# Kernel optimization log

Hardware: AMD Instinct MI355X
Metric: run time of the kernel (lower is better)

The kernel has to match this reference:

```python
import jax, jax.numpy as jnp
import numpy as np

D = 512      # n_embd
H = 8        # n_head
L = 2        # n_layer (per stack)
T = 2048     # sequence length / block_size
B = 1        # batch
BANDS = (999, 9)  # band_width for [phase, tool] stacks
EPS = 1e-5


def _sinusoidal(n_pos, dim):
    pos = np.arange(n_pos)[:, None].astype(np.float64)
    j = np.arange(dim)[None, :]
    angle = pos / np.power(10000.0, 2 * (j // 2) / dim)
    out = np.zeros((n_pos, dim), np.float32)
    out[:, 0::2] = np.sin(angle[:, 0::2])
    out[:, 1::2] = np.cos(angle[:, 1::2])
    return jnp.asarray(out)


def setup_inputs() -> dict:
    key = jax.random.key(0)
    ks = jax.random.split(key, 8)
    s = 0.02
    rn = lambda k, shp: jax.random.normal(k, shp, jnp.float32) * s
    inp = {
        "x": jax.random.normal(ks[0], (B, T, D), jnp.float32),
        "pos_emb": _sinusoidal(T, D),            # sinusoidal, frozen
        # leading dim 2 = [phase stack, tool stack], then layer dim L
        "ln1_w": jnp.ones((2, L, D)), "ln1_b": jnp.zeros((2, L, D)),
        "ln2_w": jnp.ones((2, L, D)), "ln2_b": jnp.zeros((2, L, D)),
        "Wq": rn(ks[1], (2, L, D, D)), "bq": jnp.zeros((2, L, D)),
        "Wk": rn(ks[2], (2, L, D, D)), "bk": jnp.zeros((2, L, D)),
        "Wv": rn(ks[3], (2, L, D, D)), "bv": jnp.zeros((2, L, D)),
        "Wo": rn(ks[4], (2, L, D, D)), "bo": jnp.zeros((2, L, D)),
        "W1": rn(ks[5], (2, L, D, 2 * D)), "b1": jnp.zeros((2, L, 2 * D)),
        "W2": rn(ks[6], (2, L, 2 * D, D)), "b2": jnp.zeros((2, L, D)),
        "lnf_w": jnp.ones((D,)), "lnf_b": jnp.zeros((D,)),
    }
    return inp


def _ln(x, w, b):
    mu = x.mean(-1, keepdims=True)
    var = ((x - mu) ** 2).mean(-1, keepdims=True)
    return (x - mu) / jnp.sqrt(var + EPS) * w + b


def _attn(x, Wq, bq, Wk, bk, Wv, bv, Wo, bo, bw):
    Bx, Tx, _ = x.shape
    Dh = D // H
    heads = lambda W, b: (x @ W + b).reshape(Bx, Tx, H, Dh).transpose(0, 2, 1, 3)
    q, k, v = heads(Wq, bq), heads(Wk, bk), heads(Wv, bv)
    att = jnp.einsum('bhqd,bhkd->bhqk', q, k) / jnp.sqrt(jnp.float32(Dh))
    i = jnp.arange(Tx)[:, None]
    j = jnp.arange(Tx)[None, :]
    mask = (j <= i) & (j >= i - bw)  # causal band
    att = jnp.where(mask, att, -jnp.inf)
    att = jax.nn.softmax(att, axis=-1)
    y = jnp.einsum('bhqk,bhkd->bhqd', att, v).transpose(0, 2, 1, 3).reshape(Bx, Tx, D)
    return y @ Wo + bo


def reference(x, pos_emb, ln1_w, ln1_b, ln2_w, ln2_b,
              Wq, bq, Wk, bk, Wv, bv, Wo, bo,
              W1, b1, W2, b2, lnf_w, lnf_b):
    Tx = x.shape[1]
    h0 = x + pos_emb[None, :Tx]
    outs = []
    for s in range(2):  # phase stack, tool stack
        bw = BANDS[s]
        h = h0
        for l in range(L):
            h = h + _attn(_ln(h, ln1_w[s, l], ln1_b[s, l]),
                          Wq[s, l], bq[s, l], Wk[s, l], bk[s, l],
                          Wv[s, l], bv[s, l], Wo[s, l], bo[s, l], bw)
            hm = _ln(h, ln2_w[s, l], ln2_b[s, l])
            h = h + (jax.nn.gelu(hm @ W1[s, l] + b1[s, l], approximate=False)
                     @ W2[s, l] + b2[s, l])
        outs.append(_ln(h, lnf_w, lnf_b))
    return (outs[0], outs[1])
```

## Files before the change

### kernel.cpp

```cpp
#include <hip/hip_runtime.h>
#include <stdint.h>

#define T 2048
#define D 512
#define NH 8
#define DH 64
#define L 2

typedef float floatx4 __attribute__((ext_vector_type(4)));
typedef short shortx8 __attribute__((ext_vector_type(8)));
typedef unsigned short u16;
typedef unsigned short u16x4 __attribute__((ext_vector_type(4)));

__device__ __forceinline__ u16 f2bf(float f) {
    union { float f; uint32_t u; } c; c.f = f;
    uint32_t u = c.u;
    u += 0x7fffu + ((u >> 16) & 1u);
    return (u16)(u >> 16);
}

__device__ __forceinline__ float bf2f(u16 v) {
    union { uint32_t u; float f; } c; c.u = ((uint32_t)v) << 16;
    return c.f;
}

__device__ __forceinline__ void load_lds16(const void* g, void* l) {
    __builtin_amdgcn_global_load_lds((const __attribute__((address_space(1))) void*)g,
                                     (__attribute__((address_space(3))) void*)l,
                                     16, 0, 0);
}

struct TransJobs {
    const float* src[6];
    u16* dst[6];
    const float* x;
    const float* pos;
    u16* h;
};

__global__ __launch_bounds__(256) void pre_kernel(TransJobs j) {
    __shared__ float tile[32][33];
    int tid = threadIdx.x;
    if (blockIdx.z == 24) {
        int idx = (blockIdx.y * 32 + blockIdx.x) * 256 + tid;
        float4 xv = ((const float4*)j.x)[idx];
        float4 pv = ((const float4*)j.pos)[idx];
        u16x4 hh;
        hh[0] = f2bf(xv.x + pv.x); hh[1] = f2bf(xv.y + pv.y);
        hh[2] = f2bf(xv.z + pv.z); hh[3] = f2bf(xv.w + pv.w);
        ((u16x4*)j.h)[idx] = hh;
        ((u16x4*)j.h)[idx + (T * D / 4)] = hh;
        return;
    }
    int m = blockIdx.z >> 2, slice = blockIdx.z & 3;
    int R = (m == 5) ? 1024 : 512;
    int C = (m == 4) ? 1024 : 512;
    if (blockIdx.x * 32 >= C || blockIdx.y * 32 >= R) return;
    const float* in = j.src[m] + (size_t)slice * R * C;
    u16* out = j.dst[m] + (size_t)slice * R * C;
    int tx = tid & 31, ty = tid >> 5;
    int x = blockIdx.x * 32 + tx;
    int y0 = blockIdx.y * 32;
#pragma unroll
    for (int i = 0; i < 4; i++)
        tile[ty + i * 8][tx] = in[(size_t)(y0 + ty + i * 8) * C + x];
    __syncthreads();
    int ox = y0 + tx;
#pragma unroll
    for (int i = 0; i < 4; i++)
        out[(size_t)(blockIdx.x * 32 + ty + i * 8) * R + ox] = f2bf(tile[tx][ty + i * 8]);
}

__global__ __launch_bounds__(256) void ln_res_kernel(u16* __restrict__ h,
                                                     const u16* __restrict__ part,
                                                     const float* __restrict__ wp,
                                                     const float* __restrict__ bp,
                                                     u16* __restrict__ out, int l) {
    int row = blockIdx.x * 4 + (threadIdx.x >> 6);
    int lane = threadIdx.x & 63;
    int s = row >> 11;
    int c0 = lane * 4;
    u16* xr = h + (size_t)row * D;
    u16x4 h0 = *(const u16x4*)(xr + c0);
    u16x4 h1 = *(const u16x4*)(xr + c0 + 256);
    float4 v0, v1;
    v0.x = bf2f(h0[0]); v0.y = bf2f(h0[1]); v0.z = bf2f(h0[2]); v0.w = bf2f(h0[3]);
    v1.x = bf2f(h1[0]); v1.y = bf2f(h1[1]); v1.z = bf2f(h1[2]); v1.w = bf2f(h1[3]);
    if (part) {
        const u16* p0r = part + (size_t)s * 2 * T * D + (size_t)(row & (T - 1)) * D;
        const u16* p1r = p0r + (size_t)T * D;
        u16x4 a0 = *(const u16x4*)(p0r + c0), a1 = *(const u16x4*)(p0r + c0 + 256);
        u16x4 e0 = *(const u16x4*)(p1r + c0), e1 = *(const u16x4*)(p1r + c0 + 256);
        v0.x += bf2f(a0[0]) + bf2f(e0[0]); v0.y += bf2f(a0[1]) + bf2f(e0[1]);
        v0.z += bf2f(a0[2]) + bf2f(e0[2]); v0.w += bf2f(a0[3]) + bf2f(e0[3]);
        v1.x += bf2f(a1[0]) + bf2f(e1[0]); v1.y += bf2f(a1[1]) + bf2f(e1[1]);
        v1.z += bf2f(a1[2]) + bf2f(e1[2]); v1.w += bf2f(a1[3]) + bf2f(e1[3]);
        u16x4 s0, s1;
        s0[0] = f2bf(v0.x); s0[1] = f2bf(v0.y); s0[2] = f2bf(v0.z); s0[3] = f2bf(v0.w);
        s1[0] = f2bf(v1.x); s1[1] = f2bf(v1.y); s1[2] = f2bf(v1.z); s1[3] = f2bf(v1.w);
        *(u16x4*)(xr + c0) = s0;
        *(u16x4*)(xr + c0 + 256) = s1;
    }
    float sum = v0.x + v0.y + v0.z + v0.w + v1.x + v1.y + v1.z + v1.w;
    float sq = v0.x*v0.x + v0.y*v0.y + v0.z*v0.z + v0.w*v0.w
             + v1.x*v1.x + v1.y*v1.y + v1.z*v1.z + v1.w*v1.w;
#pragma unroll
    for (int d2 = 1; d2 < 64; d2 <<= 1) { sum += __shfl_xor(sum, d2); sq += __shfl_xor(sq, d2); }
    float mu = sum * (1.0f / D);
    float var = sq * (1.0f / D) - mu * mu;
    float rstd = rsqrtf(var + 1e-5f);
    const float* w = wp + (size_t)(s * L + l) * D;
    const float* b = bp + (size_t)(s * L + l) * D;
    u16x4 p0, p1;
#pragma unroll
    for (int jj = 0; jj < 4; jj++) {
        float a = (jj == 0 ? v0.x : jj == 1 ? v0.y : jj == 2 ? v0.z : v0.w);
        p0[jj] = f2bf((a - mu) * rstd * w[c0 + jj] + b[c0 + jj]);
        float c = (jj == 0 ? v1.x : jj == 1 ? v1.y : jj == 2 ? v1.z : v1.w);
        p1[jj] = f2bf((c - mu) * rstd * w[c0 + 256 + jj] + b[c0 + 256 + jj]);
    }
    *(u16x4*)(out + (size_t)row * D + c0) = p0;
    *(u16x4*)(out + (size_t)row * D + c0 + 256) = p1;
}

__global__ __launch_bounds__(256) void lnf_kernel(const u16* __restrict__ h,
                                                  const u16* __restrict__ part,
                                                  const float* __restrict__ w,
                                                  const float* __restrict__ b,
                                                  float* __restrict__ out) {
    int row = blockIdx.x * 4 + (threadIdx.x >> 6);
    int lane = threadIdx.x & 63;
    int s = row >> 11;
    int c0 = lane * 4;
    const u16* xr = h + (size_t)row * D;
    u16x4 h0 = *(const u16x4*)(xr + c0);
    u16x4 h1 = *(const u16x4*)(xr + c0 + 256);
    float4 v0, v1;
    v0.x = bf2f(h0[0]); v0.y = bf2f(h0[1]); v0.z = bf2f(h0[2]); v0.w = bf2f(h0[3]);
    v1.x = bf2f(h1[0]); v1.y = bf2f(h1[1]); v1.z = bf2f(h1[2]); v1.w = bf2f(h1[3]);
    const u16* p0r = part + (size_t)s * 2 * T * D + (size_t)(row & (T - 1)) * D;
    const u16* p1r = p0r + (size_t)T * D;
    u16x4 a0 = *(const u16x4*)(p0r + c0), a1 = *(const u16x4*)(p0r + c0 + 256);
    u16x4 e0 = *(const u16x4*)(p1r + c0), e1 = *(const u16x4*)(p1r + c0 + 256);
    v0.x += bf2f(a0[0]) + bf2f(e0[0]); v0.y += bf2f(a0[1]) + bf2f(e0[1]);
    v0.z += bf2f(a0[2]) + bf2f(e0[2]); v0.w += bf2f(a0[3]) + bf2f(e0[3]);
    v1.x += bf2f(a1[0]) + bf2f(e1[0]); v1.y += bf2f(a1[1]) + bf2f(e1[1]);
    v1.z += bf2f(a1[2]) + bf2f(e1[2]); v1.w += bf2f(a1[3]) + bf2f(e1[3]);
    float sum = v0.x + v0.y + v0.z + v0.w + v1.x + v1.y + v1.z + v1.w;
    float sq = v0.x*v0.x + v0.y*v0.y + v0.z*v0.z + v0.w*v0.w
             + v1.x*v1.x + v1.y*v1.y + v1.z*v1.z + v1.w*v1.w;
#pragma unroll
    for (int d2 = 1; d2 < 64; d2 <<= 1) { sum += __shfl_xor(sum, d2); sq += __shfl_xor(sq, d2); }
    float mu = sum * (1.0f / D);
    float var = sq * (1.0f / D) - mu * mu;
    float rstd = rsqrtf(var + 1e-5f);
    float4 r0, r1;
    r0.x = (v0.x - mu) * rstd * w[c0+0] + b[c0+0];
    r0.y = (v0.y - mu) * rstd * w[c0+1] + b[c0+1];
    r0.z = (v0.z - mu) * rstd * w[c0+2] + b[c0+2];
    r0.w = (v0.w - mu) * rstd * w[c0+3] + b[c0+3];
    r1.x = (v1.x - mu) * rstd * w[c0+256+0] + b[c0+256+0];
    r1.y = (v1.y - mu) * rstd * w[c0+256+1] + b[c0+256+1];
    r1.z = (v1.z - mu) * rstd * w[c0+256+2] + b[c0+256+2];
    r1.w = (v1.w - mu) * rstd * w[c0+256+3] + b[c0+256+3];
    *(float4*)(out + (size_t)row * D + c0) = r0;
    *(float4*)(out + (size_t)row * D + c0 + 256) = r1;
}

struct GemmPtrs {
    const u16* A[6];
    const u16* Bt[6];
    const float* bias[6];
    void* C[6];
};

#define EPI_QKV  0
#define EPI_GELU 1
#define EPI_PART 2

template <int EPI>
__global__ __launch_bounds__(256) void gemm_kernel(GemmPtrs p, int M, int N, int K, int KS) {
    __shared__ __align__(16) u16 lA[2][64 * 32];
    __shared__ __align__(16) u16 lB[2][64 * 32];
    int nchunk = K / KS;
    int pidx = blockIdx.z / nchunk;
    int kc = blockIdx.z % nchunk;
    int koff = kc * KS;
    const u16* A = p.A[pidx];
    const u16* Bt = p.Bt[pidx];
    int m0 = blockIdx.y * 64, n0 = blockIdx.x * 64;
    int tid = threadIdx.x;
    int lane = tid & 63, wave = tid >> 6;
    int wx = wave & 1, wy = wave >> 1;
    int l16 = lane & 15, q4 = lane >> 4;
    const u16* ag = A + (size_t)(m0 + (tid >> 2)) * K + koff + (tid & 3) * 8;
    const u16* bg = Bt + (size_t)(n0 + (tid >> 2)) * K + koff + (tid & 3) * 8;
    floatx4 acc[2][2] = {};
    for (int k0 = 0; k0 < KS; k0 += 64) {
        __syncthreads();
#pragma unroll
        for (int kh = 0; kh < 2; kh++) {
            load_lds16(ag + k0 + kh * 32, &lA[kh][tid * 8]);
            load_lds16(bg + k0 + kh * 32, &lB[kh][tid * 8]);
        }
        __syncthreads();
#pragma unroll
        for (int kh = 0; kh < 2; kh++) {
            shortx8 af[2], bf[2];
#pragma unroll
            for (int t = 0; t < 2; t++) {
                af[t] = *(const shortx8*)(&lA[kh][(wy * 32 + t * 16 + l16) * 32 + q4 * 8]);
                bf[t] = *(const shortx8*)(&lB[kh][(wx * 32 + t * 16 + l16) * 32 + q4 * 8]);
            }
#pragma unroll
            for (int i = 0; i < 2; i++)
#pragma unroll
                for (int j = 0; j < 2; j++)
                    acc[i][j] = __builtin_amdgcn_mfma_f32_16x16x32_bf16(af[i], bf[j], acc[i][j], 0, 0, 0);
        }
    }
    const float* bias = p.bias[pidx];
    bool vtrans = (EPI == EPI_QKV) && (pidx % 3 == 2);
#pragma unroll
    for (int i = 0; i < 2; i++) {
        int row0 = m0 + wy * 32 + i * 16 + q4 * 4;
#pragma unroll
        for (int j = 0; j < 2; j++) {
            int col = n0 + wx * 32 + j * 16 + l16;
            float bz = (kc == 0) ? bias[col] : 0.0f;
            floatx4 a = acc[i][j];
            if (EPI == EPI_QKV) {
                if (vtrans) {
                    u16x4 pk;
#pragma unroll
                    for (int r = 0; r < 4; r++) pk[r] = f2bf(a[r] + bz);
                    *(u16x4*)((u16*)p.C[pidx] + (size_t)col * M + row0) = pk;
                } else {
#pragma unroll
                    for (int r = 0; r < 4; r++)
                        ((u16*)p.C[pidx])[(size_t)(row0 + r) * N + col] = f2bf(a[r] + bz);
                }
            } else if (EPI == EPI_GELU) {
#pragma unroll
                for (int r = 0; r < 4; r++) {
                    float v = a[r] + bz;
                    float g = 0.5f * v * (1.0f + erff(v * 0.70710678118f));
                    ((u16*)p.C[pidx])[(size_t)(row0 + r) * N + col] = f2bf(g);
                }
            } else {
#pragma unroll
                for (int r = 0; r < 4; r++)
                    ((u16*)p.C[pidx])[(size_t)kc * M * N + (size_t)(row0 + r) * N + col] = f2bf(a[r] + bz);
            }
        }
    }
}

__global__ __launch_bounds__(256) void attn_kernel(const u16* __restrict__ qg,
                                                   const u16* __restrict__ kg,
                                                   const u16* __restrict__ vtg,
                                                   u16* __restrict__ ao,
                                                   int bw0, int bw1) {
    __shared__ __align__(16) u16 pbuf[4][16 * 32];
    __shared__ float cl[4][16];
    __shared__ float co[4][16][64];
    int s = blockIdx.z, hh = blockIdx.y, q0 = blockIdx.x * 16;
    int bw = (s == 0) ? bw0 : bw1;
    int tid = threadIdx.x, wave = tid >> 6, lane = tid & 63;
    int l16 = lane & 15, q4 = lane >> 4;
    const u16* Q = qg + (size_t)s * T * D;
    const u16* Kp = kg + (size_t)s * T * D;
    const u16* V = vtg + (size_t)s * D * T;
    int hd = hh * DH;
    shortx8 qf0 = *(const shortx8*)(Q + (size_t)(q0 + l16) * D + hd + q4 * 8);
    shortx8 qf1 = *(const shortx8*)(Q + (size_t)(q0 + l16) * D + hd + 32 + q4 * 8);
    floatx4 o[4] = {};
    float lsum[4] = {};
    int klo = q0 - bw; if (klo < 0) klo = 0; klo &= ~31;
    int khi = q0 + 15;
    u16* pw = pbuf[wave];
    int kt0 = klo + wave * 32;
    shortx8 kf0, kf1, kf2, kf3, vf0, vf1, vf2, vf3;
    if (kt0 <= khi) {
        kf0 = *(const shortx8*)(Kp + (size_t)(kt0 + l16) * D + hd + q4 * 8);
        kf1 = *(const shortx8*)(Kp + (size_t)(kt0 + l16) * D + hd + 32 + q4 * 8);
        kf2 = *(const shortx8*)(Kp + (size_t)(kt0 + 16 + l16) * D + hd + q4 * 8);
        kf3 = *(const shortx8*)(Kp + (size_t)(kt0 + 16 + l16) * D + hd + 32 + q4 * 8);
        vf0 = *(const shortx8*)(V + (size_t)(hd + 0 * 16 + l16) * T + kt0 + q4 * 8);
        vf1 = *(const shortx8*)(V + (size_t)(hd + 1 * 16 + l16) * T + kt0 + q4 * 8);
        vf2 = *(const shortx8*)(V + (size_t)(hd + 2 * 16 + l16) * T + kt0 + q4 * 8);
        vf3 = *(const shortx8*)(V + (size_t)(hd + 3 * 16 + l16) * T + kt0 + q4 * 8);
    }
    for (int kt = kt0; kt <= khi; kt += 128) {
        floatx4 s0 = {}, s1 = {};
        s0 = __builtin_amdgcn_mfma_f32_16x16x32_bf16(qf0, kf0, s0, 0, 0, 0);
        s0 = __builtin_amdgcn_mfma_f32_16x16x32_bf16(qf1, kf1, s0, 0, 0, 0);
        s1 = __builtin_amdgcn_mfma_f32_16x16x32_bf16(qf0, kf2, s1, 0, 0, 0);
        s1 = __builtin_amdgcn_mfma_f32_16x16x32_bf16(qf1, kf3, s1, 0, 0, 0);
        int ktn = kt + 128;
        shortx8 nk0, nk1, nk2, nk3, nv0, nv1, nv2, nv3;
        if (ktn <= khi) {
            nk0 = *(const shortx8*)(Kp + (size_t)(ktn + l16) * D + hd + q4 * 8);
            nk1 = *(const shortx8*)(Kp + (size_t)(ktn + l16) * D + hd + 32 + q4 * 8);
            nk2 = *(const shortx8*)(Kp + (size_t)(ktn + 16 + l16) * D + hd + q4 * 8);
            nk3 = *(const shortx8*)(Kp + (size_t)(ktn + 16 + l16) * D + hd + 32 + q4 * 8);
            nv0 = *(const shortx8*)(V + (size_t)(hd + 0 * 16 + l16) * T + ktn + q4 * 8);
            nv1 = *(const shortx8*)(V + (size_t)(hd + 1 * 16 + l16) * T + ktn + q4 * 8);
            nv2 = *(const shortx8*)(V + (size_t)(hd + 2 * 16 + l16) * T + ktn + q4 * 8);
            nv3 = *(const shortx8*)(V + (size_t)(hd + 3 * 16 + l16) * T + ktn + q4 * 8);
        }
#pragma unroll
        for (int r = 0; r < 4; r++) {
            int row = q0 + q4 * 4 + r;
            int c0 = kt + l16, c1 = kt + 16 + l16;
            float p0 = (c0 <= row && c0 >= row - bw) ? __expf(s0[r] * 0.125f) : 0.0f;
            float p1 = (c1 <= row && c1 >= row - bw) ? __expf(s1[r] * 0.125f) : 0.0f;
            lsum[r] += p0 + p1;
            pw[(q4 * 4 + r) * 32 + l16] = f2bf(p0);
            pw[(q4 * 4 + r) * 32 + 16 + l16] = f2bf(p1);
        }
        shortx8 pf = *(const shortx8*)(pw + l16 * 32 + q4 * 8);
        o[0] = __builtin_amdgcn_mfma_f32_16x16x32_bf16(pf, vf0, o[0], 0, 0, 0);
        o[1] = __builtin_amdgcn_mfma_f32_16x16x32_bf16(pf, vf1, o[1], 0, 0, 0);
        o[2] = __builtin_amdgcn_mfma_f32_16x16x32_bf16(pf, vf2, o[2], 0, 0, 0);
        o[3] = __builtin_amdgcn_mfma_f32_16x16x32_bf16(pf, vf3, o[3], 0, 0, 0);
        kf0 = nk0; kf1 = nk1; kf2 = nk2; kf3 = nk3;
        vf0 = nv0; vf1 = nv1; vf2 = nv2; vf3 = nv3;
    }
#pragma unroll
    for (int r = 0; r < 4; r++) {
#pragma unroll
        for (int d2 = 1; d2 < 16; d2 <<= 1) lsum[r] += __shfl_xor(lsum[r], d2);
    }
    if (l16 == 0) {
#pragma unroll
        for (int r = 0; r < 4; r++) cl[wave][q4 * 4 + r] = lsum[r];
    }
#pragma unroll
    for (int n = 0; n < 4; n++)
#pragma unroll
        for (int r = 0; r < 4; r++)
            co[wave][q4 * 4 + r][n * 16 + l16] = o[n][r];
    __syncthreads();
#pragma unroll
    for (int i = 0; i < 4; i++) {
        int idx = tid + i * 256;
        int row = idx >> 6, col = idx & 63;
        float Ls = cl[0][row] + cl[1][row] + cl[2][row] + cl[3][row];
        float O = co[0][row][col] + co[1][row][col] + co[2][row][col] + co[3][row][col];
        ao[(size_t)s * T * D + (size_t)(q0 + row) * D + hd + col] = f2bf(O / Ls);
    }
}

extern "C" void kernel_launch(void* const* d_in, const int* in_sizes, int n_in,
                              void* d_out, int out_size, void* d_ws, size_t ws_size,
                              hipStream_t stream) {
    (void)in_sizes; (void)n_in; (void)out_size; (void)ws_size;
    const float* x     = (const float*)d_in[0];
    const float* pos   = (const float*)d_in[1];
    const float* ln1_w = (const float*)d_in[2];
    const float* ln1_b = (const float*)d_in[3];
    const float* ln2_w = (const float*)d_in[4];
    const float* ln2_b = (const float*)d_in[5];
    const float* Wq    = (const float*)d_in[6];
    const float* bq    = (const float*)d_in[7];
    const float* Wk    = (const float*)d_in[8];
    const float* bk    = (const float*)d_in[9];
    const float* Wv    = (const float*)d_in[10];
    const float* bv    = (const float*)d_in[11];
    const float* Wo    = (const float*)d_in[12];
    const float* bo    = (const float*)d_in[13];
    const float* W1    = (const float*)d_in[14];
    const float* b1    = (const float*)d_in[15];
    const float* W2    = (const float*)d_in[16];
    const float* b2    = (const float*)d_in[17];
    const float* lnf_w = (const float*)d_in[18];
    const float* lnf_b = (const float*)d_in[19];

    char* ws = (char*)d_ws;
    size_t off = 0;
    auto alloc = [&](size_t bytes) { void* p = ws + off; off += (bytes + 255) & ~(size_t)255; return p; };
    u16* WqT = (u16*)alloc((size_t)4 * 512 * 512 * 2);
    u16* WkT = (u16*)alloc((size_t)4 * 512 * 512 * 2);
    u16* WvT = (u16*)alloc((size_t)4 * 512 * 512 * 2);
    u16* WoT = (u16*)alloc((size_t)4 * 512 * 512 * 2);
    u16* W1T = (u16*)alloc((size_t)4 * 512 * 1024 * 2);
    u16* W2T = (u16*)alloc((size_t)4 * 1024 * 512 * 2);
    u16* h   = (u16*)alloc((size_t)2 * T * D * 2);
    u16* xln = (u16*)alloc((size_t)2 * T * D * 2);
    u16* qb  = (u16*)alloc((size_t)2 * T * D * 2);
    u16* kb  = (u16*)alloc((size_t)2 * T * D * 2);
    u16* vt  = (u16*)alloc((size_t)2 * T * D * 2);
    u16* ao  = (u16*)alloc((size_t)2 * T * D * 2);
    u16* ff  = (u16*)alloc((size_t)2 * T * 1024 * 2);
    u16* pp = (u16*)alloc((size_t)2 * 2 * T * D * 2);
    u16* pf = (u16*)alloc((size_t)2 * 2 * T * D * 2);

    TransJobs tj;
    tj.src[0] = Wq; tj.dst[0] = WqT;
    tj.src[1] = Wk; tj.dst[1] = WkT;
    tj.src[2] = Wv; tj.dst[2] = WvT;
    tj.src[3] = Wo; tj.dst[3] = WoT;
    tj.src[4] = W1; tj.dst[4] = W1T;
    tj.src[5] = W2; tj.dst[5] = W2T;
    tj.x = x; tj.pos = pos; tj.h = h;
    pre_kernel<<<dim3(32, 32, 25), 256, 0, stream>>>(tj);

    for (int l = 0; l < L; l++) {
        ln_res_kernel<<<(2 * T) / 4, 256, 0, stream>>>(h, l == 0 ? nullptr : pf,
                                                       ln1_w, ln1_b, xln, l);

        GemmPtrs g{};
        for (int s = 0; s < 2; s++) {
            int wo = s * L + l;
            const u16* a = xln + (size_t)s * T * D;
            g.A[s * 3 + 0] = a; g.Bt[s * 3 + 0] = WqT + (size_t)wo * 512 * 512;
            g.bias[s * 3 + 0] = bq + (size_t)wo * 512; g.C[s * 3 + 0] = qb + (size_t)s * T * D;
            g.A[s * 3 + 1] = a; g.Bt[s * 3 + 1] = WkT + (size_t)wo * 512 * 512;
            g.bias[s * 3 + 1] = bk + (size_t)wo * 512; g.C[s * 3 + 1] = kb + (size_t)s * T * D;
            g.A[s * 3 + 2] = a; g.Bt[s * 3 + 2] = WvT + (size_t)wo * 512 * 512;
            g.bias[s * 3 + 2] = bv + (size_t)wo * 512; g.C[s * 3 + 2] = vt + (size_t)s * T * D;
        }
        gemm_kernel<EPI_QKV><<<dim3(8, 32, 6), 256, 0, stream>>>(g, T, 512, 512, 512);

        attn_kernel<<<dim3(128, 8, 2), 256, 0, stream>>>(qb, kb, vt, ao, 999, 9);

        GemmPtrs gp{};
        for (int s = 0; s < 2; s++) {
            int wo = s * L + l;
            gp.A[s] = ao + (size_t)s * T * D;
            gp.Bt[s] = WoT + (size_t)wo * 512 * 512;
            gp.bias[s] = bo + (size_t)wo * 512;
            gp.C[s] = pp + (size_t)s * 2 * T * D;
        }
        gemm_kernel<EPI_PART><<<dim3(8, 32, 4), 256, 0, stream>>>(gp, T, 512, 512, 256);

        ln_res_kernel<<<(2 * T) / 4, 256, 0, stream>>>(h, pp, ln2_w, ln2_b, xln, l);

        GemmPtrs g1{};
        for (int s = 0; s < 2; s++) {
            int wo = s * L + l;
            g1.A[s] = xln + (size_t)s * T * D;
            g1.Bt[s] = W1T + (size_t)wo * 512 * 1024;
            g1.bias[s] = b1 + (size_t)wo * 1024;
            g1.C[s] = ff + (size_t)s * T * 1024;
        }
        gemm_kernel<EPI_GELU><<<dim3(16, 32, 2), 256, 0, stream>>>(g1, T, 1024, 512, 512);

        GemmPtrs g2{};
        for (int s = 0; s < 2; s++) {
            int wo = s * L + l;
            g2.A[s] = ff + (size_t)s * T * 1024;
            g2.Bt[s] = W2T + (size_t)wo * 1024 * 512;
            g2.bias[s] = b2 + (size_t)wo * 512;
            g2.C[s] = pf + (size_t)s * 2 * T * D;
        }
        gemm_kernel<EPI_PART><<<dim3(8, 32, 4), 256, 0, stream>>>(g2, T, 512, 1024, 512);
    }

    lnf_kernel<<<(2 * T) / 4, 256, 0, stream>>>(h, pf, lnf_w, lnf_b, (float*)d_out);
}
```

Measured before the change: 319.8 us.

## Stage V-transpose epilogue through LDS and widen attention query tile to 32

The QKV GEMM epilogue for V now transposes the output tile through shared memory so each thread writes two contiguous 16-byte chunks, replacing scattered 8-byte transposed stores. The attention kernel processes 32 query rows per block instead of 16, so each K/V fragment load feeds two query groups and half as many blocks are launched. The explicit register prefetch of the next K/V tile is removed, and the cross-wave reduction now accumulates in shared memory in two stages. This cuts global loads of K/V and uncoalesced stores, but may expose more load latency and lower parallelism for the short-band stack.

```diff
diff --git a/kernel.cpp b/kernel.cpp
--- a/kernel.cpp
+++ b/kernel.cpp
@@ -180,8 +180,9 @@
 
 template <int EPI>
 __global__ __launch_bounds__(256) void gemm_kernel(GemmPtrs p, int M, int N, int K, int KS) {
-    __shared__ __align__(16) u16 lA[2][64 * 32];
-    __shared__ __align__(16) u16 lB[2][64 * 32];
+    __shared__ __align__(16) u16 smem[8192];
+    u16* lA = smem;
+    u16* lB = smem + 4096;
     int nchunk = K / KS;
     int pidx = blockIdx.z / nchunk;
     int kc = blockIdx.z % nchunk;
@@ -200,8 +201,8 @@
         __syncthreads();
 #pragma unroll
         for (int kh = 0; kh < 2; kh++) {
-            load_lds16(ag + k0 + kh * 32, &lA[kh][tid * 8]);
-            load_lds16(bg + k0 + kh * 32, &lB[kh][tid * 8]);
+            load_lds16(ag + k0 + kh * 32, lA + kh * 2048 + tid * 8);
+            load_lds16(bg + k0 + kh * 32, lB + kh * 2048 + tid * 8);
         }
         __syncthreads();
 #pragma unroll
@@ -209,8 +210,8 @@
             shortx8 af[2], bf[2];
 #pragma unroll
             for (int t = 0; t < 2; t++) {
-                af[t] = *(const shortx8*)(&lA[kh][(wy * 32 + t * 16 + l16) * 32 + q4 * 8]);
-                bf[t] = *(const shortx8*)(&lB[kh][(wx * 32 + t * 16 + l16) * 32 + q4 * 8]);
+                af[t] = *(const shortx8*)(lA + kh * 2048 + (wy * 32 + t * 16 + l16) * 32 + q4 * 8);
+                bf[t] = *(const shortx8*)(lB + kh * 2048 + (wx * 32 + t * 16 + l16) * 32 + q4 * 8);
             }
 #pragma unroll
             for (int i = 0; i < 2; i++)
@@ -220,7 +221,30 @@
         }
     }
     const float* bias = p.bias[pidx];
-    bool vtrans = (EPI == EPI_QKV) && (pidx % 3 == 2);
+    if (EPI == EPI_QKV && (pidx % 3 == 2)) {
+        __syncthreads();
+#pragma unroll
+        for (int i = 0; i < 2; i++) {
+            int tl = wy * 32 + i * 16 + q4 * 4;
+#pragma unroll
+            for (int j = 0; j < 2; j++) {
+                int dl = wx * 32 + j * 16 + l16;
+                float bz = (kc == 0) ? bias[n0 + dl] : 0.0f;
+                u16x4 pk;
+#pragma unroll
+                for (int r = 0; r < 4; r++) pk[r] = f2bf(acc[i][j][r] + bz);
+                *(u16x4*)(smem + dl * 72 + tl) = pk;
+            }
+        }
+        __syncthreads();
+        int dl = tid >> 2, tc = (tid & 3) * 16;
+        u16* dst = (u16*)p.C[pidx] + (size_t)(n0 + dl) * M + m0 + tc;
+        shortx8 w0 = *(const shortx8*)(smem + dl * 72 + tc);
+        shortx8 w1 = *(const shortx8*)(smem + dl * 72 + tc + 8);
+        *(shortx8*)dst = w0;
+        *(shortx8*)(dst + 8) = w1;
+        return;
+    }
 #pragma unroll
     for (int i = 0; i < 2; i++) {
         int row0 = m0 + wy * 32 + i * 16 + q4 * 4;
@@ -230,16 +254,9 @@
             float bz = (kc == 0) ? bias[col] : 0.0f;
             floatx4 a = acc[i][j];
             if (EPI == EPI_QKV) {
-                if (vtrans) {
-                    u16x4 pk;
-#pragma unroll
-                    for (int r = 0; r < 4; r++) pk[r] = f2bf(a[r] + bz);
-                    *(u16x4*)((u16*)p.C[pidx] + (size_t)col * M + row0) = pk;
-                } else {
-#pragma unroll
-                    for (int r = 0; r < 4; r++)
-                        ((u16*)p.C[pidx])[(size_t)(row0 + r) * N + col] = f2bf(a[r] + bz);
-                }
+#pragma unroll
+                for (int r = 0; r < 4; r++)
+                    ((u16*)p.C[pidx])[(size_t)(row0 + r) * N + col] = f2bf(a[r] + bz);
             } else if (EPI == EPI_GELU) {
 #pragma unroll
                 for (int r = 0; r < 4; r++) {
@@ -261,10 +278,10 @@
                                                    const u16* __restrict__ vtg,
                                                    u16* __restrict__ ao,
                                                    int bw0, int bw1) {
-    __shared__ __align__(16) u16 pbuf[4][16 * 32];
-    __shared__ float cl[4][16];
-    __shared__ float co[4][16][64];
-    int s = blockIdx.z, hh = blockIdx.y, q0 = blockIdx.x * 16;
+    __shared__ __align__(16) u16 pbuf[4][32 * 32];
+    __shared__ float cl[2][32];
+    __shared__ float co[2][32][64];
+    int s = blockIdx.z, hh = blockIdx.y, q0 = blockIdx.x * 32;
     int bw = (s == 0) ? bw0 : bw1;
     int tid = threadIdx.x, wave = tid >> 6, lane = tid & 63;
     int l16 = lane & 15, q4 = lane >> 4;
@@ -272,82 +289,104 @@
     const u16* Kp = kg + (size_t)s * T * D;
     const u16* V = vtg + (size_t)s * D * T;
     int hd = hh * DH;
-    shortx8 qf0 = *(const shortx8*)(Q + (size_t)(q0 + l16) * D + hd + q4 * 8);
-    shortx8 qf1 = *(const shortx8*)(Q + (size_t)(q0 + l16) * D + hd + 32 + q4 * 8);
-    floatx4 o[4] = {};
-    float lsum[4] = {};
+    shortx8 qf[2][2];
+#pragma unroll
+    for (int g = 0; g < 2; g++)
+#pragma unroll
+        for (int hf = 0; hf < 2; hf++)
+            qf[g][hf] = *(const shortx8*)(Q + (size_t)(q0 + g * 16 + l16) * D + hd + hf * 32 + q4 * 8);
+    floatx4 o[2][4] = {};
+    float lsum[2][4] = {};
     int klo = q0 - bw; if (klo < 0) klo = 0; klo &= ~31;
-    int khi = q0 + 15;
+    int khi = q0 + 31;
     u16* pw = pbuf[wave];
-    int kt0 = klo + wave * 32;
-    shortx8 kf0, kf1, kf2, kf3, vf0, vf1, vf2, vf3;
-    if (kt0 <= khi) {
-        kf0 = *(const shortx8*)(Kp + (size_t)(kt0 + l16) * D + hd + q4 * 8);
-        kf1 = *(const shortx8*)(Kp + (size_t)(kt0 + l16) * D + hd + 32 + q4 * 8);
-        kf2 = *(const shortx8*)(Kp + (size_t)(kt0 + 16 + l16) * D + hd + q4 * 8);
-        kf3 = *(const shortx8*)(Kp + (size_t)(kt0 + 16 + l16) * D + hd + 32 + q4 * 8);
-        vf0 = *(const shortx8*)(V + (size_t)(hd + 0 * 16 + l16) * T + kt0 + q4 * 8);
-        vf1 = *(const shortx8*)(V + (size_t)(hd + 1 * 16 + l16) * T + kt0 + q4 * 8);
-        vf2 = *(const shortx8*)(V + (size_t)(hd + 2 * 16 + l16) * T + kt0 + q4 * 8);
-        vf3 = *(const shortx8*)(V + (size_t)(hd + 3 * 16 + l16) * T + kt0 + q4 * 8);
-    }
-    for (int kt = kt0; kt <= khi; kt += 128) {
-        floatx4 s0 = {}, s1 = {};
-        s0 = __builtin_amdgcn_mfma_f32_16x16x32_bf16(qf0, kf0, s0, 0, 0, 0);
-        s0 = __builtin_amdgcn_mfma_f32_16x16x32_bf16(qf1, kf1, s0, 0, 0, 0);
-        s1 = __builtin_amdgcn_mfma_f32_16x16x32_bf16(qf0, kf2, s1, 0, 0, 0);
-        s1 = __builtin_amdgcn_mfma_f32_16x16x32_bf16(qf1, kf3, s1, 0, 0, 0);
-        int ktn = kt + 128;
-        shortx8 nk0, nk1, nk2, nk3, nv0, nv1, nv2, nv3;
-        if (ktn <= khi) {
-            nk0 = *(const shortx8*)(Kp + (size_t)(ktn + l16) * D + hd + q4 * 8);
-            nk1 = *(const shortx8*)(Kp + (size_t)(ktn + l16) * D + hd + 32 + q4 * 8);
-            nk2 = *(const shortx8*)(Kp + (size_t)(ktn + 16 + l16) * D + hd + q4 * 8);
-            nk3 = *(const shortx8*)(Kp + (size_t)(ktn + 16 + l16) * D + hd + 32 + q4 * 8);
-            nv0 = *(const shortx8*)(V + (size_t)(hd + 0 * 16 + l16) * T + ktn + q4 * 8);
-            nv1 = *(const shortx8*)(V + (size_t)(hd + 1 * 16 + l16) * T + ktn + q4 * 8);
-            nv2 = *(const shortx8*)(V + (size_t)(hd + 2 * 16 + l16) * T + ktn + q4 * 8);
-            nv3 = *(const shortx8*)(V + (size_t)(hd + 3 * 16 + l16) * T + ktn + q4 * 8);
-        }
+    for (int kt = klo + wave * 32; kt <= khi; kt += 128) {
+        shortx8 vf[4];
+#pragma unroll
+        for (int n = 0; n < 4; n++)
+            vf[n] = *(const shortx8*)(V + (size_t)(hd + n * 16 + l16) * T + kt + q4 * 8);
+        shortx8 kf[2][2];
+#pragma unroll
+        for (int t = 0; t < 2; t++)
+#pragma unroll
+            for (int hf = 0; hf < 2; hf++)
+                kf[t][hf] = *(const shortx8*)(Kp + (size_t)(kt + t * 16 + l16) * D + hd + hf * 32 + q4 * 8);
+        floatx4 sc[2][2] = {};
+#pragma unroll
+        for (int g = 0; g < 2; g++)
+#pragma unroll
+            for (int t = 0; t < 2; t++) {
+                sc[g][t] = __builtin_amdgcn_mfma_f32_16x16x32_bf16(qf[g][0], kf[t][0], sc[g][t], 0, 0, 0);
+                sc[g][t] = __builtin_amdgcn_mfma_f32_16x16x32_bf16(qf[g][1], kf[t][1], sc[g][t], 0, 0, 0);
+            }
+#pragma unroll
+        for (int g = 0; g < 2; g++)
+#pragma unroll
+            for (int r = 0; r < 4; r++) {
+                int row = q0 + g * 16 + q4 * 4 + r;
+#pragma unroll
+                for (int t = 0; t < 2; t++) {
+                    int c = kt + t * 16 + l16;
+                    float pv = (c <= row && c >= row - bw) ? __expf(sc[g][t][r] * 0.125f) : 0.0f;
+                    lsum[g][r] += pv;
+                    pw[(g * 16 + q4 * 4 + r) * 32 + t * 16 + l16] = f2bf(pv);
+                }
+            }
+        shortx8 pf[2];
+#pragma unroll
+        for (int g = 0; g < 2; g++)
+            pf[g] = *(const shortx8*)(pw + (g * 16 + l16) * 32 + q4 * 8);
+#pragma unroll
+        for (int g = 0; g < 2; g++)
+#pragma unroll
+            for (int n = 0; n < 4; n++)
+                o[g][n] = __builtin_amdgcn_mfma_f32_16x16x32_bf16(pf[g], vf[n], o[g][n], 0, 0, 0);
+    }
+#pragma unroll
+    for (int g = 0; g < 2; g++)
 #pragma unroll
         for (int r = 0; r < 4; r++) {
-            int row = q0 + q4 * 4 + r;
-            int c0 = kt + l16, c1 = kt + 16 + l16;
-            float p0 = (c0 <= row && c0 >= row - bw) ? __expf(s0[r] * 0.125f) : 0.0f;
-            float p1 = (c1 <= row && c1 >= row - bw) ? __expf(s1[r] * 0.125f) : 0.0f;
-            lsum[r] += p0 + p1;
-            pw[(q4 * 4 + r) * 32 + l16] = f2bf(p0);
-            pw[(q4 * 4 + r) * 32 + 16 + l16] = f2bf(p1);
-        }
-        shortx8 pf = *(const shortx8*)(pw + l16 * 32 + q4 * 8);
-        o[0] = __builtin_amdgcn_mfma_f32_16x16x32_bf16(pf, vf0, o[0], 0, 0, 0);
-        o[1] = __builtin_amdgcn_mfma_f32_16x16x32_bf16(pf, vf1, o[1], 0, 0, 0);
-        o[2] = __builtin_amdgcn_mfma_f32_16x16x32_bf16(pf, vf2, o[2], 0, 0, 0);
-        o[3] = __builtin_amdgcn_mfma_f32_16x16x32_bf16(pf, vf3, o[3], 0, 0, 0);
-        kf0 = nk0; kf1 = nk1; kf2 = nk2; kf3 = nk3;
-        vf0 = nv0; vf1 = nv1; vf2 = nv2; vf3 = nv3;
-    }
-#pragma unroll
-    for (int r = 0; r < 4; r++) {
-#pragma unroll
-        for (int d2 = 1; d2 < 16; d2 <<= 1) lsum[r] += __shfl_xor(lsum[r], d2);
-    }
-    if (l16 == 0) {
-#pragma unroll
-        for (int r = 0; r < 4; r++) cl[wave][q4 * 4 + r] = lsum[r];
-    }
-#pragma unroll
-    for (int n = 0; n < 4; n++)
-#pragma unroll
-        for (int r = 0; r < 4; r++)
-            co[wave][q4 * 4 + r][n * 16 + l16] = o[n][r];
+#pragma unroll
+            for (int d2 = 1; d2 < 16; d2 <<= 1) lsum[g][r] += __shfl_xor(lsum[g][r], d2);
+        }
+    if (wave >= 2) {
+        if (l16 == 0) {
+#pragma unroll
+            for (int g = 0; g < 2; g++)
+#pragma unroll
+                for (int r = 0; r < 4; r++) cl[wave - 2][g * 16 + q4 * 4 + r] = lsum[g][r];
+        }
+#pragma unroll
+        for (int g = 0; g < 2; g++)
+#pragma unroll
+            for (int n = 0; n < 4; n++)
+#pragma unroll
+                for (int r = 0; r < 4; r++)
+                    co[wave - 2][g * 16 + q4 * 4 + r][n * 16 + l16] = o[g][n][r];
+    }
     __syncthreads();
-#pragma unroll
-    for (int i = 0; i < 4; i++) {
+    if (wave < 2) {
+        if (l16 == 0) {
+#pragma unroll
+            for (int g = 0; g < 2; g++)
+#pragma unroll
+                for (int r = 0; r < 4; r++) cl[wave][g * 16 + q4 * 4 + r] += lsum[g][r];
+        }
+#pragma unroll
+        for (int g = 0; g < 2; g++)
+#pragma unroll
+            for (int n = 0; n < 4; n++)
+#pragma unroll
+                for (int r = 0; r < 4; r++)
+                    co[wave][g * 16 + q4 * 4 + r][n * 16 + l16] += o[g][n][r];
+    }
+    __syncthreads();
+#pragma unroll
+    for (int i = 0; i < 8; i++) {
         int idx = tid + i * 256;
         int row = idx >> 6, col = idx & 63;
-        float Ls = cl[0][row] + cl[1][row] + cl[2][row] + cl[3][row];
-        float O = co[0][row][col] + co[1][row][col] + co[2][row][col] + co[3][row][col];
+        float Ls = cl[0][row] + cl[1][row];
+        float O = co[0][row][col] + co[1][row][col];
         ao[(size_t)s * T * D + (size_t)(q0 + row) * D + hd + col] = f2bf(O / Ls);
     }
 }
@@ -423,7 +462,7 @@
         }
         gemm_kernel<EPI_QKV><<<dim3(8, 32, 6), 256, 0, stream>>>(g, T, 512, 512, 512);
 
-        attn_kernel<<<dim3(128, 8, 2), 256, 0, stream>>>(qb, kb, vt, ao, 999, 9);
+        attn_kernel<<<dim3(64, 8, 2), 256, 0, stream>>>(qb, kb, vt, ao, 999, 9);
 
         GemmPtrs gp{};
         for (int s = 0; s < 2; s++) {
```

Result: faster. 294.9 us (-7.8%).
